# Performance work log

Hardware: AMD Instinct MI355X
Metric: run time of the kernel (lower is better)

## Reference

```python
import jax, jax.numpy as jnp
import numpy as np

D_IN = 1024
D_MODEL = 1024
NUM_HEADS = 16
DEPTH = D_MODEL // NUM_HEADS


def setup_inputs() -> dict:
    key = jax.random.key(0)
    ks = jax.random.split(key, 7)
    B, N = 2, 2048
    s = 1.0 / np.sqrt(D_IN)
    return {
        "x": jax.random.normal(ks[0], (B, N, D_IN), dtype=jnp.float32),
        "Wq": jax.random.normal(ks[1], (D_IN, D_MODEL), dtype=jnp.float32) * s,
        "bq": jnp.zeros((D_MODEL,), dtype=jnp.float32),
        "Wk": jax.random.normal(ks[2], (D_IN, D_MODEL), dtype=jnp.float32) * s,
        "bk": jnp.zeros((D_MODEL,), dtype=jnp.float32),
        "Wv": jax.random.normal(ks[3], (D_IN, D_MODEL), dtype=jnp.float32) * s,
        "bv": jnp.zeros((D_MODEL,), dtype=jnp.float32),
    }


def _split_heads(t):
    B, N, _ = t.shape
    return t.reshape(B, N, NUM_HEADS, DEPTH).transpose(0, 2, 1, 3)  # [B,H,N,depth]


def reference(x, Wq, bq, Wk, bk, Wv, bv):
    B, N, _ = x.shape
    q = _split_heads(x @ Wq + bq)
    k = _split_heads(x @ Wk + bk)
    v = _split_heads(x @ Wv + bv)
    scale = 1.0 / jnp.sqrt(jnp.float32(DEPTH))
    attn = jnp.einsum("bhnd,bhmd->bhnm", q, k) * scale  # [B,H,N,N]
    attn = jax.nn.softmax(attn, axis=-1)
    out = jnp.einsum("bhnm,bhmd->bhnd", attn, v)
    return out.transpose(0, 2, 1, 3).reshape(B, N, D_MODEL)
```

## Files before the change

kernel.cpp:

```cpp
#include <hip/hip_runtime.h>
#include <cstdint>


#define SEQ_N 2048
#define NHEAD 16
#define DEPTH 64
#define SCALE_Q (0.125f * 1.44269504088896340736f)
#define M_OFF (-12.0f)

typedef short bf16x8 __attribute__((ext_vector_type(8)));
typedef short short4v __attribute__((ext_vector_type(4)));
typedef float f32x4 __attribute__((ext_vector_type(4)));

#define MFMA32(a, b, c) __builtin_amdgcn_mfma_f32_16x16x32_bf16((a), (b), (c), 0, 0, 0)

#if defined(__has_builtin)
#if __has_builtin(__builtin_amdgcn_exp2f)
#define FEXP2(x) __builtin_amdgcn_exp2f(x)
#endif
#endif
#ifndef FEXP2
#define FEXP2(x) exp2f(x)
#endif

__device__ __forceinline__ short f2b(float f) {
    union { float f; unsigned u; } v; v.f = f;
    unsigned u = v.u;
    return (short)((u + 0x7FFFu + ((u >> 16) & 1u)) >> 16);
}

__device__ __forceinline__ unsigned cvt_pk_bf16(float lo, float hi) {
    unsigned r;
    asm("v_cvt_pk_bf16_f32 %0, %1, %2" : "=v"(r) : "v"(lo), "v"(hi));
    return r;
}

__device__ __forceinline__ void gld_lds16(const void* g, void* l) {
    __builtin_amdgcn_global_load_lds(
        (const __attribute__((address_space(1))) unsigned int*)(uintptr_t)g,
        (__attribute__((address_space(3))) unsigned int*)(uintptr_t)l, 16, 0, 0);
}

__global__ __launch_bounds__(256) void cvt_all_kernel(
    const float* __restrict__ x, short* __restrict__ xb,
    const float* __restrict__ Wq, const float* __restrict__ Wk,
    const float* __restrict__ Wv, short* __restrict__ WT)
{
    __shared__ float tile[64][65];
    if (blockIdx.x < 2048) {
        const int i = blockIdx.x * 256 + threadIdx.x;
        const float4* xi = (const float4*)x + (size_t)i * 2;
        const float4 a = xi[0], c = xi[1];
        bf16x8 o;
        o[0] = f2b(a.x); o[1] = f2b(a.y); o[2] = f2b(a.z); o[3] = f2b(a.w);
        o[4] = f2b(c.x); o[5] = f2b(c.y); o[6] = f2b(c.z); o[7] = f2b(c.w);
        *((bf16x8*)xb + i) = o;
        return;
    }
    const int bid = blockIdx.x - 2048;
    const int mat = bid >> 8;
    const int t = bid & 255;
    const int k0 = (t >> 4) * 64, n0 = (t & 15) * 64;
    const float* W = (mat == 0) ? Wq : ((mat == 1) ? Wk : Wv);
    const int tt = threadIdx.x;
#pragma unroll
    for (int i = 0; i < 16; ++i) {
        const int idx = tt + i * 256;
        const int r = idx >> 6, c = idx & 63;
        tile[r][c] = W[(size_t)(k0 + r) * 1024 + n0 + c];
    }
    __syncthreads();
#pragma unroll
    for (int i = 0; i < 16; ++i) {
        const int idx = tt + i * 256;
        const int r = idx >> 6, c = idx & 63;
        WT[(size_t)(mat * 1024 + n0 + r) * 1024 + k0 + c] = f2b(tile[c][r]);
    }
}

#define GEMM_K 1024

__global__ __launch_bounds__(512, 2) void qkv_gemm_kernel(
    const short* __restrict__ A, const short* __restrict__ BT,
    const float* __restrict__ bq, const float* __restrict__ bk, const float* __restrict__ bv,
    short* __restrict__ Qb, short* __restrict__ Kb, short* __restrict__ VTb)
{
    __shared__ __align__(16) short sm[57344];
    const int tid = threadIdx.x;
    const int l = tid & 63, w = tid >> 6;
    const int lr = l & 15, lk = l >> 4;
    const int wr = w >> 2, wcn = w & 3;

    const int id2 = (blockIdx.x & 7) * 32 + (blockIdx.x >> 3);
    const int bm = id2 & 15, bn = id2 >> 4;
    const int row0 = bm * 256, col0 = bn * 192;

    const int gsrc8 = ((tid & 7) ^ ((tid >> 3) & 7)) << 3;
    const short* a_src = A + (size_t)(row0 + (tid >> 3)) * 1024 + gsrc8;
    const short* b_src = BT + (size_t)(col0 + (tid >> 3)) * 1024 + gsrc8;

    const int aBase = (wr * 128 + lr) * 64;
    const int bBase = (wcn * 48 + lr) * 64;
    const int asw0 = ((lk)     ^ (lr & 7)) << 3;
    const int asw1 = ((lk + 4) ^ (lr & 7)) << 3;

    f32x4 acc[8][3];
#pragma unroll
    for (int m = 0; m < 8; ++m)
#pragma unroll
        for (int n = 0; n < 3; ++n) acc[m][n] = (f32x4){0.f, 0.f, 0.f, 0.f};

    gld_lds16(a_src,          sm + tid * 8);
    gld_lds16(a_src + 65536,  sm + tid * 8 + 4096);
    gld_lds16(a_src + 131072, sm + tid * 8 + 8192);
    gld_lds16(a_src + 196608, sm + tid * 8 + 12288);
    gld_lds16(b_src,          sm + 32768 + tid * 8);
    gld_lds16(b_src + 65536,  sm + 32768 + tid * 8 + 4096);
    gld_lds16(b_src + 131072, sm + 32768 + tid * 8 + 8192);

#define PHASE(P, GLDS)                                                          \
    do {                                                                        \
        bf16x8 af[2][2];                                                        \
        af[0][0] = *(const bf16x8*)(Al + aBase + (2*(P))*1024 + asw0);          \
        af[0][1] = *(const bf16x8*)(Al + aBase + (2*(P))*1024 + asw1);          \
        af[1][0] = *(const bf16x8*)(Al + aBase + (2*(P)+1)*1024 + asw0);        \
        af[1][1] = *(const bf16x8*)(Al + aBase + (2*(P)+1)*1024 + asw1);        \
        GLDS;                                                                   \
        __builtin_amdgcn_s_barrier();                                           \
        asm volatile("s_waitcnt lgkmcnt(0)" ::: "memory");                      \
        __builtin_amdgcn_sched_barrier(0);                                      \
        __builtin_amdgcn_s_setprio(1);                                          \
        _Pragma("unroll")                                                       \
        for (int mm = 0; mm < 2; ++mm)                                          \
            _Pragma("unroll")                                                   \
            for (int n = 0; n < 3; ++n) {                                       \
                acc[2*(P)+mm][n] = MFMA32(af[mm][0], bfv[n][0], acc[2*(P)+mm][n]); \
                acc[2*(P)+mm][n] = MFMA32(af[mm][1], bfv[n][1], acc[2*(P)+mm][n]); \
            }                                                                   \
        __builtin_amdgcn_s_setprio(0);                                          \
        __builtin_amdgcn_s_barrier();                                           \
    } while (0)

#pragma unroll 2
    for (int kt = 0; kt < 16; ++kt) {
        const int cur = kt & 1, nxt = cur ^ 1;
        const short* Al = sm + cur * 16384;
        const short* Bl = sm + 32768 + cur * 12288;
        short* And = sm + nxt * 16384;
        short* Bnd = sm + 32768 + nxt * 12288;
        const int k1 = (kt + 1) * 64;
        const bool more = (kt < 15);

        bf16x8 bfv[3][2];

        if (more) {
            gld_lds16(a_src + k1,         And + tid * 8);
            gld_lds16(a_src + k1 + 65536, And + tid * 8 + 4096);
            asm volatile("s_waitcnt vmcnt(2)" ::: "memory");
        } else {
            asm volatile("s_waitcnt vmcnt(0)" ::: "memory");
        }
        __builtin_amdgcn_s_barrier();
        __builtin_amdgcn_sched_barrier(0);
        {
            bf16x8 af[2][2];
            af[0][0] = *(const bf16x8*)(Al + aBase + asw0);
            af[0][1] = *(const bf16x8*)(Al + aBase + asw1);
            af[1][0] = *(const bf16x8*)(Al + aBase + 1024 + asw0);
            af[1][1] = *(const bf16x8*)(Al + aBase + 1024 + asw1);
#pragma unroll
            for (int n = 0; n < 3; ++n) {
                bfv[n][0] = *(const bf16x8*)(Bl + bBase + n * 1024 + asw0);
                bfv[n][1] = *(const bf16x8*)(Bl + bBase + n * 1024 + asw1);
            }
            asm volatile("s_waitcnt lgkmcnt(0)" ::: "memory");
            __builtin_amdgcn_sched_barrier(0);
            __builtin_amdgcn_s_setprio(1);
#pragma unroll
            for (int mm = 0; mm < 2; ++mm)
#pragma unroll
                for (int n = 0; n < 3; ++n) {
                    acc[mm][n] = MFMA32(af[mm][0], bfv[n][0], acc[mm][n]);
                    acc[mm][n] = MFMA32(af[mm][1], bfv[n][1], acc[mm][n]);
                }
            __builtin_amdgcn_s_setprio(0);
        }
        __builtin_amdgcn_s_barrier();

        PHASE(1, if (more) { gld_lds16(a_src + k1 + 131072, And + tid * 8 + 8192);
                             gld_lds16(a_src + k1 + 196608, And + tid * 8 + 12288); });
        PHASE(2, if (more) { gld_lds16(b_src + k1,          Bnd + tid * 8);
                             gld_lds16(b_src + k1 + 65536,  Bnd + tid * 8 + 4096); });
        PHASE(3, if (more) { gld_lds16(b_src + k1 + 131072, Bnd + tid * 8 + 8192); });
    }
#undef PHASE

    short* Cl = sm;
#pragma unroll
    for (int n = 0; n < 3; ++n) {
        const int gb = col0 + wcn * 48 + n * 16;
        const int mat = gb >> 10;
        const int jj = (gb + lr) & 1023;
        if (mat < 2) {
            const float bias = ((mat == 0) ? bq : bk)[jj];
            const float sc = (mat == 0) ? SCALE_Q : 1.0f;
            const int cc = wcn * 48 + n * 16 + lr;
#pragma unroll
            for (int m = 0; m < 8; ++m) {
                const int rbase = wr * 128 + m * 16 + lk * 4;
#pragma unroll
                for (int r = 0; r < 4; ++r)
                    Cl[(rbase + r) * 200 + cc] = f2b((acc[m][n][r] + bias) * sc);
            }
        } else {
            const float bias = bv[jj];
            const int h = jj >> 6, d = jj & 63;
#pragma unroll
            for (int m = 0; m < 8; ++m) {
                const int grow0 = row0 + wr * 128 + m * 16 + lk * 4;
                const int bb = grow0 >> 11, ns0 = grow0 & 2047;
                const int g = (ns0 >> 2) & 15;
                const int gp = (g & 8) | ((g & 3) << 1) | ((g >> 2) & 1);
                const int nsp = (ns0 & ~63) | (gp << 2);
                short4v pv;
#pragma unroll
                for (int r = 0; r < 4; ++r) pv[r] = f2b(acc[m][n][r] + bias);
                *(short4v*)(VTb + ((size_t)(bb * NHEAD + h) * DEPTH + d) * SEQ_N + nsp) = pv;
            }
        }
    }
    __syncthreads();
    {
        const int row = tid >> 1, half = tid & 1;
        const int grow = row0 + row;
        const int bb = grow >> 11, ns = grow & 2047;
#pragma unroll
        for (int i = 0; i < 12; ++i) {
            const int cc = half * 96 + i * 8;
            const int gc = col0 + cc;
            const int mat = gc >> 10;
            if (mat < 2) {
                short* O = mat ? Kb : Qb;
                const int h = (gc & 1023) >> 6, d0 = gc & 63;
                *(bf16x8*)(O + ((size_t)(bb * NHEAD + h) * SEQ_N + ns) * DEPTH + d0) =
                    *(const bf16x8*)(Cl + row * 200 + cc);
            }
        }
    }
}


__device__ __forceinline__ float exppack32_lane(const f32x4 s[4], bf16x8 pb[2]) {
    float rs = 0.f;
#pragma unroll
    for (int kk = 0; kk < 2; ++kk) {
        union { unsigned u[4]; bf16x8 v; } pk;
#pragma unroll
        for (int hh = 0; hh < 2; ++hh) {
            const int c = 2 * kk + hh;
            const float p0 = FEXP2(s[c][0]);
            const float p1 = FEXP2(s[c][1]);
            const float p2 = FEXP2(s[c][2]);
            const float p3 = FEXP2(s[c][3]);
            rs += (p0 + p1) + (p2 + p3);
            pk.u[2 * hh]     = cvt_pk_bf16(p0, p1);
            pk.u[2 * hh + 1] = cvt_pk_bf16(p2, p3);
        }
        pb[kk] = pk.v;
    }
    return rs;
}

#define NTK 16

__global__ __launch_bounds__(256, 2) void attn_kernel(
    const short* __restrict__ Qb, const short* __restrict__ Kb,
    const short* __restrict__ VTb, float* __restrict__ out)
{
    __shared__ __align__(16) short smem[2][2][8192];

    const int tid = threadIdx.x;
    const int l = tid & 63, w = tid >> 6;
    const int lr = l & 15, lk = l >> 4;
    const int qh = w & 1, kh = w >> 1;

    const int hb = blockIdx.x;
    const int slot = hb >> 3;
    const int bh = (hb & 7) * 4 + (slot >> 4);
    const int qt = slot & 15;
    const int b = bh >> 4, h = bh & 15;

    const int qw = qt * 128 + qh * 64;

    const short* Qg = Qb + ((size_t)bh * SEQ_N + qw + lr) * DEPTH + lk * 8;
    bf16x8 bq[4][2];
#pragma unroll
    for (int g = 0; g < 4; ++g) {
        bq[g][0] = *(const bf16x8*)(Qg + g * 16 * DEPTH);
        bq[g][1] = *(const bf16x8*)(Qg + g * 16 * DEPTH + 32);
    }

    const short* Kg = Kb + (size_t)bh * SEQ_N * DEPTH;
    const short* Vg = VTb + (size_t)bh * DEPTH * SEQ_N;

    const int srow = tid >> 3;
    const int sg = (tid & 7) ^ (srow & 7);
    const short* Ksrc = Kg + (size_t)srow * DEPTH + sg * 8;
    const short* Vsrc = Vg + (size_t)srow * SEQ_N + sg * 8;

#define STAGE(BUF, T)                                                             \
    do {                                                                          \
        const int ko_ = (T) * 64;                                                 \
        short* d0 = &smem[BUF][0][w * 512];                                       \
        short* d1 = &smem[BUF][1][w * 512];                                       \
        gld_lds16(Ksrc + (size_t)ko_ * DEPTH, d0);                                \
        gld_lds16(Ksrc + (size_t)(ko_ + 32) * DEPTH, d0 + 2048);                  \
        gld_lds16(Vsrc + ko_, d0 + 4096);                                         \
        gld_lds16(Vsrc + ko_ + 32 * SEQ_N, d0 + 6144);                            \
        gld_lds16(Ksrc + (size_t)(1024 + ko_) * DEPTH, d1);                       \
        gld_lds16(Ksrc + (size_t)(1024 + ko_ + 32) * DEPTH, d1 + 2048);           \
        gld_lds16(Vsrc + 1024 + ko_, d1 + 4096);                                  \
        gld_lds16(Vsrc + 1024 + ko_ + 32 * SEQ_N, d1 + 6144);                     \
    } while (0)

    const int aoff0 = lr * 64 + (((lk    ) ^ (lr & 7)) << 3);
    const int aoff1 = lr * 64 + (((lk + 4) ^ (lr & 7)) << 3);

    f32x4 acc[4][4];
#pragma unroll
    for (int g = 0; g < 4; ++g)
#pragma unroll
        for (int n = 0; n < 4; ++n) acc[g][n] = (f32x4){0.f, 0.f, 0.f, 0.f};
    float lsum[4] = {0.f, 0.f, 0.f, 0.f};

    STAGE(0, 0);
    asm volatile("s_waitcnt vmcnt(0)" ::: "memory");
    __builtin_amdgcn_s_barrier();
    __builtin_amdgcn_sched_barrier(0);

#pragma unroll 2
    for (int t = 0; t < NTK; ++t) {
        const int cur = t & 1;
        const int tn = (t + 1 < NTK) ? (t + 1) : (NTK - 1);
        STAGE(cur ^ 1, tn);

        const short* Kl = &smem[cur][kh][0];
        const short* Vl = Kl + 4096;

        bf16x8 kf[4][2], vf[4][2];
#pragma unroll
        for (int c = 0; c < 4; ++c) {
            kf[c][0] = *(const bf16x8*)(Kl + c * 1024 + aoff0);
            kf[c][1] = *(const bf16x8*)(Kl + c * 1024 + aoff1);
        }
#pragma unroll
        for (int n = 0; n < 4; ++n) {
            vf[n][0] = *(const bf16x8*)(Vl + n * 1024 + aoff0);
            vf[n][1] = *(const bf16x8*)(Vl + n * 1024 + aoff1);
        }

#pragma unroll
        for (int g = 0; g < 4; ++g) {
            f32x4 s[4];
            __builtin_amdgcn_s_setprio(1);
#pragma unroll
            for (int c = 0; c < 4; ++c) {
                f32x4 a = (f32x4){M_OFF, M_OFF, M_OFF, M_OFF};
                a = MFMA32(kf[c][0], bq[g][0], a);
                a = MFMA32(kf[c][1], bq[g][1], a);
                s[c] = a;
            }
            __builtin_amdgcn_s_setprio(0);

            bf16x8 pb[2];
            lsum[g] += exppack32_lane(s, pb);

            __builtin_amdgcn_s_setprio(1);
#pragma unroll
            for (int n = 0; n < 4; ++n) {
                acc[g][n] = MFMA32(vf[n][0], pb[0], acc[g][n]);
                acc[g][n] = MFMA32(vf[n][1], pb[1], acc[g][n]);
            }
            __builtin_amdgcn_s_setprio(0);
        }

        asm volatile("s_waitcnt vmcnt(0)" ::: "memory");
        __builtin_amdgcn_s_barrier();
        __builtin_amdgcn_sched_barrier(0);
    }
#undef STAGE

#pragma unroll
    for (int g = 0; g < 4; ++g) {
        lsum[g] += __shfl_xor(lsum[g], 16);
        lsum[g] += __shfl_xor(lsum[g], 32);
    }

    float* fsm = (float*)&smem[0][0][0];
    const int pbase = qh * 4416;
    if (kh == 1) {
#pragma unroll
        for (int g = 0; g < 4; ++g)
#pragma unroll
            for (int n = 0; n < 4; ++n)
                *(f32x4*)(fsm + pbase + (g * 16 + lr) * 68 + n * 16 + lk * 4) = acc[g][n];
        if (lk == 0) {
#pragma unroll
            for (int g = 0; g < 4; ++g) fsm[pbase + 4352 + g * 16 + lr] = lsum[g];
        }
    }
    __syncthreads();
    if (kh == 0) {
#pragma unroll
        for (int g = 0; g < 4; ++g) {
            const float lt = lsum[g] + fsm[pbase + 4352 + g * 16 + lr];
            const float inv = 1.0f / lt;
            float* o = out + ((size_t)b * SEQ_N + qw + g * 16 + lr) * 1024 + h * 64 + lk * 4;
#pragma unroll
            for (int n = 0; n < 4; ++n) {
                const f32x4 p = *(const f32x4*)(fsm + pbase + (g * 16 + lr) * 68 + n * 16 + lk * 4);
                *(f32x4*)(o + n * 16) = (acc[g][n] + p) * inv;
            }
        }
    }
}

extern "C" void kernel_launch(void* const* d_in, const int* in_sizes, int n_in,
                              void* d_out, int out_size, void* d_ws, size_t ws_size,
                              hipStream_t stream) {
    const float* x  = (const float*)d_in[0];
    const float* Wq = (const float*)d_in[1];
    const float* bq = (const float*)d_in[2];
    const float* Wk = (const float*)d_in[3];
    const float* bk = (const float*)d_in[4];
    const float* Wv = (const float*)d_in[5];
    const float* bv = (const float*)d_in[6];
    float* out = (float*)d_out;

    char* ws = (char*)d_ws;
    short* xb  = (short*)(ws);
    short* WT  = (short*)(ws + (8  << 20));
    short* Qb  = (short*)(ws + (14 << 20));
    short* Kb  = (short*)(ws + (22 << 20));
    short* VTb = (short*)(ws + (30 << 20));

    cvt_all_kernel<<<2816, 256, 0, stream>>>(x, xb, Wq, Wk, Wv, WT);
    qkv_gemm_kernel<<<256, 512, 0, stream>>>(xb, WT, bq, bk, bv, Qb, Kb, VTb);
    attn_kernel<<<512, 256, 0, stream>>>(Qb, Kb, VTb, out);
}
```

Baseline: 83.27 us.

## Split attention block across 8 waves with 32 query rows each

Doubles the attention block size from 256 to 512 threads. Each wave now handles 32 query rows instead of 64, and the KV range is still split in two halves. K/V staging is spread across all 512 threads, and the per-wave accumulator and Q registers are halved. This targets register pressure and is meant to raise occupancy and latency hiding, at the cost of reloading each K/V fragment from LDS for fewer MFMAs (lower reuse per wave) and more waves contending at barriers.

```diff
diff --git a/kernel.cpp b/kernel.cpp
--- a/kernel.cpp
+++ b/kernel.cpp
@@ -273,7 +273,7 @@
 
 #define NTK 16
 
-__global__ __launch_bounds__(256, 2) void attn_kernel(
+__global__ __launch_bounds__(512, 4) void attn_kernel(
     const short* __restrict__ Qb, const short* __restrict__ Kb,
     const short* __restrict__ VTb, float* __restrict__ out)
 {
@@ -282,7 +282,7 @@
     const int tid = threadIdx.x;
     const int l = tid & 63, w = tid >> 6;
     const int lr = l & 15, lk = l >> 4;
-    const int qh = w & 1, kh = w >> 1;
+    const int qq = w >> 1, kh = w & 1;
 
     const int hb = blockIdx.x;
     const int slot = hb >> 3;
@@ -290,12 +290,12 @@
     const int qt = slot & 15;
     const int b = bh >> 4, h = bh & 15;
 
-    const int qw = qt * 128 + qh * 64;
+    const int qw = qt * 128 + qq * 32;
 
     const short* Qg = Qb + ((size_t)bh * SEQ_N + qw + lr) * DEPTH + lk * 8;
-    bf16x8 bq[4][2];
-#pragma unroll
-    for (int g = 0; g < 4; ++g) {
+    bf16x8 bq[2][2];
+#pragma unroll
+    for (int g = 0; g < 2; ++g) {
         bq[g][0] = *(const bf16x8*)(Qg + g * 16 * DEPTH);
         bq[g][1] = *(const bf16x8*)(Qg + g * 16 * DEPTH + 32);
     }
@@ -303,35 +303,32 @@
     const short* Kg = Kb + (size_t)bh * SEQ_N * DEPTH;
     const short* Vg = VTb + (size_t)bh * DEPTH * SEQ_N;
 
-    const int srow = tid >> 3;
-    const int sg = (tid & 7) ^ (srow & 7);
-    const short* Ksrc = Kg + (size_t)srow * DEPTH + sg * 8;
-    const short* Vsrc = Vg + (size_t)srow * SEQ_N + sg * 8;
-
-#define STAGE(BUF, T)                                                             \
-    do {                                                                          \
-        const int ko_ = (T) * 64;                                                 \
-        short* d0 = &smem[BUF][0][w * 512];                                       \
-        short* d1 = &smem[BUF][1][w * 512];                                       \
-        gld_lds16(Ksrc + (size_t)ko_ * DEPTH, d0);                                \
-        gld_lds16(Ksrc + (size_t)(ko_ + 32) * DEPTH, d0 + 2048);                  \
-        gld_lds16(Vsrc + ko_, d0 + 4096);                                         \
-        gld_lds16(Vsrc + ko_ + 32 * SEQ_N, d0 + 6144);                            \
-        gld_lds16(Ksrc + (size_t)(1024 + ko_) * DEPTH, d1);                       \
-        gld_lds16(Ksrc + (size_t)(1024 + ko_ + 32) * DEPTH, d1 + 2048);           \
-        gld_lds16(Vsrc + 1024 + ko_, d1 + 4096);                                  \
-        gld_lds16(Vsrc + 1024 + ko_ + 32 * SEQ_N, d1 + 6144);                     \
+    const int t8 = tid & 255;
+    const int half = tid >> 8;
+    const int srow = t8 >> 3;
+    const int sg = (t8 & 7) ^ (srow & 7);
+    const short* Ksrc = Kg + ((size_t)(half * 1024) + srow) * DEPTH + sg * 8;
+    const short* Vsrc = Vg + (size_t)srow * SEQ_N + half * 1024 + sg * 8;
+
+#define STAGE(BUF, T)                                                            \
+    do {                                                                         \
+        const int ko_ = (T) * 64;                                                \
+        short* dk = &smem[BUF][half][0] + t8 * 8;                                \
+        gld_lds16(Ksrc + (size_t)ko_ * DEPTH, dk);                               \
+        gld_lds16(Ksrc + (size_t)(ko_ + 32) * DEPTH, dk + 2048);                 \
+        gld_lds16(Vsrc + ko_, dk + 4096);                                        \
+        gld_lds16(Vsrc + ko_ + 32 * SEQ_N, dk + 6144);                           \
     } while (0)
 
     const int aoff0 = lr * 64 + (((lk    ) ^ (lr & 7)) << 3);
     const int aoff1 = lr * 64 + (((lk + 4) ^ (lr & 7)) << 3);
 
-    f32x4 acc[4][4];
-#pragma unroll
-    for (int g = 0; g < 4; ++g)
+    f32x4 acc[2][4];
+#pragma unroll
+    for (int g = 0; g < 2; ++g)
 #pragma unroll
         for (int n = 0; n < 4; ++n) acc[g][n] = (f32x4){0.f, 0.f, 0.f, 0.f};
-    float lsum[4] = {0.f, 0.f, 0.f, 0.f};
+    float lsum[2] = {0.f, 0.f};
 
     STAGE(0, 0);
     asm volatile("s_waitcnt vmcnt(0)" ::: "memory");
@@ -360,7 +357,7 @@
         }
 
 #pragma unroll
-        for (int g = 0; g < 4; ++g) {
+        for (int g = 0; g < 2; ++g) {
             f32x4 s[4];
             __builtin_amdgcn_s_setprio(1);
 #pragma unroll
@@ -391,29 +388,29 @@
 #undef STAGE
 
 #pragma unroll
-    for (int g = 0; g < 4; ++g) {
+    for (int g = 0; g < 2; ++g) {
         lsum[g] += __shfl_xor(lsum[g], 16);
         lsum[g] += __shfl_xor(lsum[g], 32);
     }
 
     float* fsm = (float*)&smem[0][0][0];
-    const int pbase = qh * 4416;
+    const int pbase = qq * 2208;
     if (kh == 1) {
 #pragma unroll
-        for (int g = 0; g < 4; ++g)
+        for (int g = 0; g < 2; ++g)
 #pragma unroll
             for (int n = 0; n < 4; ++n)
                 *(f32x4*)(fsm + pbase + (g * 16 + lr) * 68 + n * 16 + lk * 4) = acc[g][n];
         if (lk == 0) {
 #pragma unroll
-            for (int g = 0; g < 4; ++g) fsm[pbase + 4352 + g * 16 + lr] = lsum[g];
+            for (int g = 0; g < 2; ++g) fsm[pbase + 2176 + g * 16 + lr] = lsum[g];
         }
     }
     __syncthreads();
     if (kh == 0) {
 #pragma unroll
-        for (int g = 0; g < 4; ++g) {
-            const float lt = lsum[g] + fsm[pbase + 4352 + g * 16 + lr];
+        for (int g = 0; g < 2; ++g) {
+            const float lt = lsum[g] + fsm[pbase + 2176 + g * 16 + lr];
             const float inv = 1.0f / lt;
             float* o = out + ((size_t)b * SEQ_N + qw + g * 16 + lr) * 1024 + h * 64 + lk * 4;
 #pragma unroll
@@ -446,5 +443,5 @@
 
     cvt_all_kernel<<<2816, 256, 0, stream>>>(x, xb, Wq, Wk, Wv, WT);
     qkv_gemm_kernel<<<256, 512, 0, stream>>>(xb, WT, bq, bk, bv, Qb, Kb, VTb);
-    attn_kernel<<<512, 256, 0, stream>>>(Qb, Kb, VTb, out);
-}
+    attn_kernel<<<512, 512, 0, stream>>>(Qb, Kb, VTb, out);
+}
```

Result: slower. 237.1 us (+184.7%).
